# Performance work log

Measured on AMD Instinct MI355X. Metric: run time of the kernel, lower is better.

Reference implementation:

```python
import jax, jax.numpy as jnp
import numpy as np

B, C, H, W = 2, 512, 64, 64
NUM_HEADS = 8
HEAD_DIM = C // NUM_HEADS


def setup_inputs() -> dict:
    key = jax.random.key(0)
    ks = jax.random.split(key, 6)
    s = 1.0 / np.sqrt(C)
    return {
        "x": jax.random.normal(ks[0], (B, C, H, W), dtype=jnp.float32),
        "w_qkv": jax.random.normal(ks[1], (3 * C, C), dtype=jnp.float32) * s,
        "b_qkv": jax.random.normal(ks[2], (3 * C,), dtype=jnp.float32) * 0.01,
        "w_out": jax.random.normal(ks[3], (C, C), dtype=jnp.float32) * s,
        "b_out": jax.random.normal(ks[4], (C,), dtype=jnp.float32) * 0.01,
        "gamma": jax.random.normal(ks[5], (1,), dtype=jnp.float32) * 0.1,
    }


def reference(x, w_qkv, b_qkv, w_out, b_out, gamma):
    b, c, h, w = x.shape
    n = h * w
    nh, hd = NUM_HEADS, HEAD_DIM
    # 1x1 conv QKV projection == per-pixel linear
    qkv = jnp.einsum('oc,bchw->bohw', w_qkv, x) + b_qkv[None, :, None, None]
    qkv = qkv.reshape(b, 3, nh, hd, n)  # [B,3,nh,hd,N]
    q = qkv[:, 0].transpose(0, 1, 3, 2)  # [B,nh,N,hd]
    k = qkv[:, 1]                        # [B,nh,hd,N]
    v = qkv[:, 2].transpose(0, 1, 3, 2)  # [B,nh,N,hd]
    scale = hd ** -0.5
    attn = jnp.einsum('bhnd,bhdm->bhnm', q, k) * scale  # [B,nh,N,N]
    attn = jax.nn.softmax(attn, axis=-1)
    out = jnp.einsum('bhnm,bhmd->bhnd', attn, v)  # [B,nh,N,hd]
    out = out.transpose(0, 1, 3, 2).reshape(b, c, h, w)  # [B,C,H,W]
    out = jnp.einsum('oc,bchw->bohw', w_out, out) + b_out[None, :, None, None]
    return gamma[0] * out + x
```

## Files before the change

kernel.cpp:

```cpp
#include <hip/hip_runtime.h>
#include <hip/hip_bf16.h>

typedef __bf16 bf16_t;
typedef __bf16 bf16x8 __attribute__((ext_vector_type(8)));
typedef __bf16 bf16x4 __attribute__((ext_vector_type(4)));
typedef float floatx4 __attribute__((ext_vector_type(4)));
typedef float f32x16 __attribute__((ext_vector_type(16)));

#define MFMA_BF16(a, b, c) __builtin_amdgcn_mfma_f32_16x16x32_bf16((a), (b), (c), 0, 0, 0)
#define MFMA32(a, b, c) __builtin_amdgcn_mfma_f32_32x32x16_bf16((a), (b), (c), 0, 0, 0)

static constexpr int CB = 512;
static constexpr int NB = 4096;

__device__ __forceinline__ unsigned cvtpk_bf16(float lo, float hi_) {
  unsigned r;
  asm("v_cvt_pk_bf16_f32 %0, %1, %2" : "=v"(r) : "v"(lo), "v"(hi_));
  return r;
}
__device__ __forceinline__ void plswap(unsigned& x, unsigned& y) {
  asm volatile("v_permlane32_swap_b32 %0, %1" : "+v"(x), "+v"(y));
}
__device__ __forceinline__ float exp2_fast(float x) {
  float r;
  asm("v_exp_f32 %0, %1" : "=v"(r) : "v"(x));
  return r;
}

#define GLOAD_LDS16(gsrc, ldst)                                              \
  __builtin_amdgcn_global_load_lds(                                          \
      (const __attribute__((address_space(1))) void*)(gsrc),                 \
      (__attribute__((address_space(3))) void*)(ldst), 16, 0, 0)

__global__ __launch_bounds__(256) void k_qkv(const float* __restrict__ W,
                                             const float* __restrict__ bias,
                                             const float* __restrict__ x,
                                             bf16_t* __restrict__ Qb,
                                             bf16_t* __restrict__ Kb,
                                             bf16_t* __restrict__ Vb) {
  __shared__ __align__(16) bf16_t As[128 * 40];
  __shared__ __align__(16) bf16_t Bs[128 * 40];
  const int t = threadIdx.x;
  const int lane = t & 63, wv = t >> 6;
  const int g = lane >> 4, c = lane & 15;
  const int wm = wv >> 1, wn = wv & 1;
  const int o0 = blockIdx.x * 128, n0 = blockIdx.y * 128;
  const int b = blockIdx.z;

  floatx4 acc[4][4] = {};

  const float* Ap = W + (size_t)o0 * CB;
  const float* xb = x + (size_t)b * CB * NB + n0;

  for (int kt = 0; kt < CB; kt += 32) {
    {
      const int row = t >> 3, c4 = (t & 7) * 4;
#pragma unroll
      for (int p = 0; p < 4; ++p) {
        const int r = row + p * 32;
        const float4 v = *reinterpret_cast<const float4*>(Ap + (size_t)r * CB + kt + c4);
        bf16x4 w4;
        w4[0] = (bf16_t)v.x; w4[1] = (bf16_t)v.y; w4[2] = (bf16_t)v.z; w4[3] = (bf16_t)v.w;
        *reinterpret_cast<bf16x4*>(&As[r * 40 + c4]) = w4;
      }
    }
    {
      const int p2 = (t & 15) * 2;
      const int nq0 = t >> 4;
      const float* xr0 = xb + (size_t)(kt + p2) * NB;
      const float* xr1 = xr0 + NB;
#pragma unroll
      for (int it = 0; it < 2; ++it) {
        const int nn = (nq0 + 16 * it) * 4;
        const float4 a = *reinterpret_cast<const float4*>(xr0 + nn);
        const float4 bv = *reinterpret_cast<const float4*>(xr1 + nn);
        const unsigned u0 = cvtpk_bf16(a.x, bv.x);
        const unsigned u1 = cvtpk_bf16(a.y, bv.y);
        const unsigned u2 = cvtpk_bf16(a.z, bv.z);
        const unsigned u3 = cvtpk_bf16(a.w, bv.w);
        *reinterpret_cast<unsigned*>(&Bs[(nn + 0) * 40 + p2]) = u0;
        *reinterpret_cast<unsigned*>(&Bs[(nn + 1) * 40 + p2]) = u1;
        *reinterpret_cast<unsigned*>(&Bs[(nn + 2) * 40 + p2]) = u2;
        *reinterpret_cast<unsigned*>(&Bs[(nn + 3) * 40 + p2]) = u3;
      }
    }
    __syncthreads();
    bf16x8 af[4], bfr[4];
#pragma unroll
    for (int i = 0; i < 4; ++i)
      af[i] = *reinterpret_cast<const bf16x8*>(&As[(wm * 64 + i * 16 + c) * 40 + g * 8]);
#pragma unroll
    for (int j = 0; j < 4; ++j)
      bfr[j] = *reinterpret_cast<const bf16x8*>(&Bs[(wn * 64 + j * 16 + c) * 40 + g * 8]);
#pragma unroll
    for (int i = 0; i < 4; ++i)
#pragma unroll
      for (int j = 0; j < 4; ++j)
        acc[i][j] = MFMA_BF16(af[i], bfr[j], acc[i][j]);
    __syncthreads();
  }

  const int which = o0 >> 9;
#pragma unroll
  for (int i = 0; i < 4; ++i) {
    const int ob = o0 + wm * 64 + i * 16 + 4 * g;
    float bias4[4];
#pragma unroll
    for (int r = 0; r < 4; ++r) bias4[r] = bias[ob + r];
    const int h = (ob >> 6) & 7;
    const int d0 = ob & 63;
#pragma unroll
    for (int j = 0; j < 4; ++j) {
      const int n = n0 + wn * 64 + j * 16 + c;
      if (which == 2) {
        bf16_t* vp = Vb + (size_t)(b * 8 + h) * 64 * NB + n;
#pragma unroll
        for (int r = 0; r < 4; ++r)
          vp[(size_t)(d0 + r) * NB] = (bf16_t)(acc[i][j][r] + bias4[r]);
      } else {
        bf16_t* qp = (which == 0 ? Qb : Kb) + ((size_t)(b * 8 + h) * NB + n) * 64 + d0;
        bf16x4 pk;
#pragma unroll
        for (int r = 0; r < 4; ++r) pk[r] = (bf16_t)(acc[i][j][r] + bias4[r]);
        *reinterpret_cast<bf16x4*>(qp) = pk;
      }
    }
  }
}

__global__ __launch_bounds__(256, 2) void k_attn(const bf16_t* __restrict__ Qb,
                                                 const bf16_t* __restrict__ Kb,
                                                 const bf16_t* __restrict__ Vb,
                                                 bf16_t* __restrict__ P0,
                                                 bf16_t* __restrict__ P1,
                                                 float* __restrict__ lsum) {
  __shared__ __align__(16) bf16_t Kl[2][2][4096];
  __shared__ __align__(16) bf16_t Vl[2][2][4096];
  const int t = threadIdx.x, lane = t & 63, w = t >> 6;
  const int q31 = lane & 31, hi = lane >> 5;

  const int bid = blockIdx.x;
  const int xcd = bid & 7, j = bid >> 3;
  const int bh = xcd * 2 + (j >> 6);
  const int rest = j & 63;
  const int qt = rest >> 1, half = rest & 1;
  const int q0 = qt * 128 + w * 32;
  const int kvbase = half * 2048;

  const size_t base = (size_t)bh * NB * 64;
  const bf16_t* Qp = Qb + base;
  const bf16_t* Kp = Kb + base;
  const bf16_t* Vp = Vb + base;
  bf16_t* Op = (half ? P1 : P0) + base;

  const float SC = 0.125f * 1.44269504088896340736f;
  const float FM = 8.0f;

  bf16x8 qf[4];
#pragma unroll
  for (int ks = 0; ks < 4; ++ks) {
    bf16x8 q = *reinterpret_cast<const bf16x8*>(Qp + (size_t)(q0 + q31) * 64 + ks * 16 + hi * 8);
#pragma unroll
    for (int e = 0; e < 8; ++e) q[e] = (bf16_t)((float)q[e] * SC);
    qf[ks] = q;
  }

  bf16x8 ones;
#pragma unroll
  for (int e = 0; e < 8; ++e) ones[e] = (bf16_t)1.0f;

  const int srow0 = t >> 3, srow1 = srow0 + 32;
  const int sc0 = ((t & 7) ^ (srow0 & 7)) * 8;
  const int sc1 = ((t & 7) ^ (srow1 & 7)) * 8;
  const bf16_t* ksrc0 = Kp + (size_t)(kvbase + srow0) * 64 + sc0;
  const bf16_t* ksrc1 = Kp + (size_t)(kvbase + srow1) * 64 + sc1;
  const bf16_t* vsrc0 = Vp + (size_t)srow0 * NB + kvbase + sc0;
  const bf16_t* vsrc1 = Vp + (size_t)srow1 * NB + kvbase + sc1;

#define STAGE128(ss, bufi)                                                    \
  do {                                                                        \
    const size_t ko_ = (size_t)(ss) * 8192;                                   \
    const int vo_ = (ss) * 128;                                               \
    bf16_t* kd0_ = &Kl[(bufi)][0][0];                                         \
    bf16_t* kd1_ = &Kl[(bufi)][1][0];                                         \
    bf16_t* vd0_ = &Vl[(bufi)][0][0];                                         \
    bf16_t* vd1_ = &Vl[(bufi)][1][0];                                         \
    GLOAD_LDS16(ksrc0 + ko_, kd0_ + w * 512);                                 \
    GLOAD_LDS16(ksrc1 + ko_, kd0_ + 2048 + w * 512);                          \
    GLOAD_LDS16(ksrc0 + ko_ + 4096, kd1_ + w * 512);                          \
    GLOAD_LDS16(ksrc1 + ko_ + 4096, kd1_ + 2048 + w * 512);                   \
    GLOAD_LDS16(vsrc0 + vo_, vd0_ + w * 512);                                 \
    GLOAD_LDS16(vsrc1 + vo_, vd0_ + 2048 + w * 512);                         \
    GLOAD_LDS16(vsrc0 + vo_ + 64, vd1_ + w * 512);                            \
    GLOAD_LDS16(vsrc1 + vo_ + 64, vd1_ + 2048 + w * 512);                     \
  } while (0)

  int c16r[4];
#pragma unroll
  for (int ks = 0; ks < 4; ++ks) c16r[ks] = ((ks * 2 + hi) ^ (q31 & 7)) * 8;

  f32x16 O0 = {}, O1 = {}, lacc = {};
  f32x16 NEGM;
#pragma unroll
  for (int r = 0; r < 16; ++r) NEGM[r] = -FM;

  STAGE128(0, 0);
  asm volatile("s_waitcnt vmcnt(0)" ::: "memory");
  __builtin_amdgcn_s_barrier();
  __builtin_amdgcn_sched_barrier(0);

  int buf = 0;
  for (int s = 0; s < 16; ++s) {
    if (s < 15) STAGE128(s + 1, buf ^ 1);
#pragma unroll
    for (int sub = 0; sub < 2; ++sub) {
      const bf16_t* Kbuf = &Kl[buf][sub][0];
      const bf16_t* Vbuf = &Vl[buf][sub][0];
      f32x16 st0 = NEGM, st1 = NEGM;
      __builtin_amdgcn_s_setprio(1);
#pragma unroll
      for (int ks = 0; ks < 4; ++ks) {
        bf16x8 kf0 = *reinterpret_cast<const bf16x8*>(&Kbuf[q31 * 64 + c16r[ks]]);
        bf16x8 kf1 = *reinterpret_cast<const bf16x8*>(&Kbuf[(32 + q31) * 64 + c16r[ks]]);
        st0 = MFMA32(kf0, qf[ks], st0);
        st1 = MFMA32(kf1, qf[ks], st1);
      }
      __builtin_amdgcn_s_setprio(0);

#pragma unroll
      for (int r = 0; r < 16; ++r) st0[r] = exp2_fast(st0[r]);
#pragma unroll
      for (int r = 0; r < 16; ++r) st1[r] = exp2_fast(st1[r]);

      __builtin_amdgcn_s_setprio(1);
#pragma unroll
      for (int ks = 0; ks < 4; ++ks) {
        const f32x16& P = (ks < 2) ? st0 : st1;
        const int rb = (ks & 1) * 8;
        unsigned x0 = cvtpk_bf16(P[rb + 0], P[rb + 1]);
        unsigned y0 = cvtpk_bf16(P[rb + 4], P[rb + 5]);
        unsigned x1 = cvtpk_bf16(P[rb + 2], P[rb + 3]);
        unsigned y1 = cvtpk_bf16(P[rb + 6], P[rb + 7]);
        plswap(x0, y0);
        plswap(x1, y1);
        union { unsigned u[4]; bf16x8 v; } pa;
        pa.u[0] = x0; pa.u[1] = x1; pa.u[2] = y0; pa.u[3] = y1;
        bf16x8 vf0 = *reinterpret_cast<const bf16x8*>(&Vbuf[q31 * 64 + c16r[ks]]);
        bf16x8 vf1 = *reinterpret_cast<const bf16x8*>(&Vbuf[(32 + q31) * 64 + c16r[ks]]);
        O0 = MFMA32(pa.v, vf0, O0);
        O1 = MFMA32(pa.v, vf1, O1);
        lacc = MFMA32(pa.v, ones, lacc);
      }
      __builtin_amdgcn_s_setprio(0);
    }
    if (s < 15) {
      asm volatile("s_waitcnt vmcnt(0) lgkmcnt(0)" ::: "memory");
      __builtin_amdgcn_s_barrier();
      __builtin_amdgcn_sched_barrier(0);
    }
    buf ^= 1;
  }
#undef STAGE128

#pragma unroll
  for (int r = 0; r < 16; ++r) {
    const int n = q0 + (r & 3) + 8 * (r >> 2) + 4 * hi;
    bf16_t* op = Op + ((size_t)n) * 64 + q31;
    op[0]  = (bf16_t)O0[r];
    op[32] = (bf16_t)O1[r];
  }
  if (q31 == 0) {
    float* lp = lsum + (size_t)(half * 16 + bh) * NB;
#pragma unroll
    for (int r = 0; r < 16; ++r) {
      const int row = (r & 3) + 8 * (r >> 2) + 4 * hi;
      lp[q0 + row] = lacc[r];
    }
  }
}

__global__ __launch_bounds__(256) void k_out(const float* __restrict__ W,
                                             const float* __restrict__ bias,
                                             const bf16_t* __restrict__ P0,
                                             const bf16_t* __restrict__ P1,
                                             const float* __restrict__ lsum,
                                             const float* __restrict__ x,
                                             const float* __restrict__ gamma,
                                             float* __restrict__ y) {
  __shared__ __align__(16) bf16_t As[128 * 40];
  __shared__ __align__(16) bf16_t Bs[128 * 40];
  const int t = threadIdx.x;
  const int lane = t & 63, wv = t >> 6;
  const int g = lane >> 4, c = lane & 15;
  const int wm = wv >> 1, wn = wv & 1;
  const int o0 = blockIdx.x * 128, n0 = blockIdx.y * 128;
  const int b = blockIdx.z;

  floatx4 acc[4][4] = {};

  const float* Ap = W + (size_t)o0 * CB;

  for (int kt = 0; kt < CB; kt += 32) {
    {
      const int row = t >> 3, c4 = (t & 7) * 4;
#pragma unroll
      for (int p = 0; p < 4; ++p) {
        const int r = row + p * 32;
        const float4 v = *reinterpret_cast<const float4*>(Ap + (size_t)r * CB + kt + c4);
        bf16x4 w4;
        w4[0] = (bf16_t)v.x; w4[1] = (bf16_t)v.y; w4[2] = (bf16_t)v.z; w4[3] = (bf16_t)v.w;
        *reinterpret_cast<bf16x4*>(&As[r * 40 + c4]) = w4;
      }
    }
    {
      const int row = t >> 2, ch = t & 3;
      const int cc = kt + ch * 8;
      const int h = cc >> 6, d = cc & 63;
#pragma unroll
      for (int p = 0; p < 2; ++p) {
        const int r = row + p * 64;
        const int n = n0 + r;
        const size_t li = (size_t)(b * 8 + h) * NB + n;
        const size_t idx = li * 64 + d;
        const bf16x8 oa = *reinterpret_cast<const bf16x8*>(P0 + idx);
        const bf16x8 ob = *reinterpret_cast<const bf16x8*>(P1 + idx);
        const float rl = 1.0f / (lsum[li] + lsum[li + 16 * NB]);
        bf16x8 o;
#pragma unroll
        for (int e = 0; e < 8; ++e)
          o[e] = (bf16_t)(((float)oa[e] + (float)ob[e]) * rl);
        *reinterpret_cast<bf16x8*>(&Bs[r * 40 + ch * 8]) = o;
      }
    }
    __syncthreads();
    bf16x8 af[4], bfr[4];
#pragma unroll
    for (int i = 0; i < 4; ++i)
      af[i] = *reinterpret_cast<const bf16x8*>(&As[(wm * 64 + i * 16 + c) * 40 + g * 8]);
#pragma unroll
    for (int j = 0; j < 4; ++j)
      bfr[j] = *reinterpret_cast<const bf16x8*>(&Bs[(wn * 64 + j * 16 + c) * 40 + g * 8]);
#pragma unroll
    for (int i = 0; i < 4; ++i)
#pragma unroll
      for (int j = 0; j < 4; ++j)
        acc[i][j] = MFMA_BF16(af[i], bfr[j], acc[i][j]);
    __syncthreads();
  }

  const float gm = gamma[0];
#pragma unroll
  for (int i = 0; i < 4; ++i) {
    const int ob = o0 + wm * 64 + i * 16 + 4 * g;
    float bias4[4];
#pragma unroll
    for (int r = 0; r < 4; ++r) bias4[r] = bias[ob + r];
#pragma unroll
    for (int j = 0; j < 4; ++j) {
      const int n = n0 + wn * 64 + j * 16 + c;
      const float* xp = x + ((size_t)(b * CB + ob) * NB) + n;
      float* yp = y + ((size_t)(b * CB + ob) * NB) + n;
#pragma unroll
      for (int r = 0; r < 4; ++r)
        yp[(size_t)r * NB] = gm * (acc[i][j][r] + bias4[r]) + xp[(size_t)r * NB];
    }
  }
}

extern "C" void kernel_launch(void* const* d_in, const int* in_sizes, int n_in,
                              void* d_out, int out_size, void* d_ws, size_t ws_size,
                              hipStream_t stream) {
  const float* x      = (const float*)d_in[0];
  const float* w_qkv  = (const float*)d_in[1];
  const float* b_qkv  = (const float*)d_in[2];
  const float* w_out  = (const float*)d_in[3];
  const float* b_out  = (const float*)d_in[4];
  const float* gamma  = (const float*)d_in[5];
  float* y = (float*)d_out;

  const size_t CH = 4194304;
  bf16_t* Wp = (bf16_t*)d_ws;
  bf16_t* Qb = Wp;
  bf16_t* Kb = Wp + CH;
  bf16_t* Vb = Wp + 2 * CH;
  bf16_t* P0 = Wp + 3 * CH;
  bf16_t* P1 = Wp + 4 * CH;
  float*  lsum = (float*)(Wp + 5 * CH);

  k_qkv<<<dim3(12, 32, 2), 256, 0, stream>>>(w_qkv, b_qkv, x, Qb, Kb, Vb);
  k_attn<<<dim3(1024), 256, 0, stream>>>(Qb, Kb, Vb, P0, P1, lsum);
  k_out<<<dim3(4, 32, 2), 256, 0, stream>>>(w_out, b_out, P0, P1, lsum, x, gamma, y);
}
```

Baseline: 155.9 us.

## Pre-convert weights and transpose x to bf16, double-buffer QKV GEMM with direct LDS loads

Adds a kernel that converts both weight matrices to bf16 once per call and a kernel that transposes x into a bf16 [B,N,C] layout. The QKV GEMM then streams both operands with global_load_lds into double-buffered, XOR-swizzled LDS tiles with a K-step of 64, overlapping loads with MFMA work. The output projection also loads pre-converted bf16 weights directly into LDS. This removes per-tile fp32 loads and conversion from the GEMM inner loops, at the cost of two extra launches and extra workspace traffic. xT shares workspace with P0, which is safe only because k_qkv finishes before k_attn writes P0.

```diff
diff --git a/kernel.cpp b/kernel.cpp
--- a/kernel.cpp
+++ b/kernel.cpp
@@ -32,73 +32,124 @@
       (const __attribute__((address_space(1))) void*)(gsrc),                 \
       (__attribute__((address_space(3))) void*)(ldst), 16, 0, 0)
 
-__global__ __launch_bounds__(256) void k_qkv(const float* __restrict__ W,
-                                             const float* __restrict__ bias,
-                                             const float* __restrict__ x,
-                                             bf16_t* __restrict__ Qb,
-                                             bf16_t* __restrict__ Kb,
-                                             bf16_t* __restrict__ Vb) {
-  __shared__ __align__(16) bf16_t As[128 * 40];
-  __shared__ __align__(16) bf16_t Bs[128 * 40];
+__global__ __launch_bounds__(256) void k_cvtw(const float* __restrict__ w_qkv,
+                                              const float* __restrict__ w_out,
+                                              bf16_t* __restrict__ Wb,
+                                              bf16_t* __restrict__ Wo) {
+  const int idx = (blockIdx.x * 256 + threadIdx.x) * 8;
+  const float* src;
+  bf16_t* dst;
+  if (idx < 786432) { src = w_qkv + idx; dst = Wb + idx; }
+  else              { src = w_out + (idx - 786432); dst = Wo + (idx - 786432); }
+  const float4 a = *reinterpret_cast<const float4*>(src);
+  const float4 b = *reinterpret_cast<const float4*>(src + 4);
+  union { unsigned u[4]; bf16x8 v; } o;
+  o.u[0] = cvtpk_bf16(a.x, a.y);
+  o.u[1] = cvtpk_bf16(a.z, a.w);
+  o.u[2] = cvtpk_bf16(b.x, b.y);
+  o.u[3] = cvtpk_bf16(b.z, b.w);
+  *reinterpret_cast<bf16x8*>(dst) = o.v;
+}
+
+__global__ __launch_bounds__(256) void k_transpose(const float* __restrict__ x,
+                                                   bf16_t* __restrict__ xT) {
+  __shared__ __align__(16) bf16_t T[64 * 72];
   const int t = threadIdx.x;
-  const int lane = t & 63, wv = t >> 6;
+  const int b = blockIdx.z, c0 = blockIdx.y * 64, n0 = blockIdx.x * 64;
+  {
+    const int cl = t >> 4, nl = (t & 15) * 4;
+#pragma unroll
+    for (int p = 0; p < 4; ++p) {
+      const int c = cl + p * 16;
+      const float4 v = *reinterpret_cast<const float4*>(
+          x + ((size_t)(b * CB + c0 + c) * NB) + n0 + nl);
+      T[(nl + 0) * 72 + c] = (bf16_t)v.x;
+      T[(nl + 1) * 72 + c] = (bf16_t)v.y;
+      T[(nl + 2) * 72 + c] = (bf16_t)v.z;
+      T[(nl + 3) * 72 + c] = (bf16_t)v.w;
+    }
+  }
+  __syncthreads();
+  {
+    const int nr = t >> 2, ch = t & 3;
+    bf16_t* op = xT + ((size_t)(b * NB + n0 + nr) * CB) + c0;
+#pragma unroll
+    for (int p = 0; p < 2; ++p) {
+      bf16x8 v = *reinterpret_cast<const bf16x8*>(&T[nr * 72 + ch * 8 + p * 32]);
+      *reinterpret_cast<bf16x8*>(op + ch * 8 + p * 32) = v;
+    }
+  }
+}
+
+__global__ __launch_bounds__(256, 2) void k_qkv(const bf16_t* __restrict__ Wb,
+                                                const float* __restrict__ bias,
+                                                const bf16_t* __restrict__ xT,
+                                                bf16_t* __restrict__ Qb,
+                                                bf16_t* __restrict__ Kb,
+                                                bf16_t* __restrict__ Vb) {
+  __shared__ __align__(16) bf16_t As[2][128 * 64];
+  __shared__ __align__(16) bf16_t Bs[2][128 * 64];
+  const int t = threadIdx.x, lane = t & 63, w = t >> 6;
   const int g = lane >> 4, c = lane & 15;
-  const int wm = wv >> 1, wn = wv & 1;
+  const int wm = w >> 1, wn = w & 1;
   const int o0 = blockIdx.x * 128, n0 = blockIdx.y * 128;
   const int b = blockIdx.z;
 
   floatx4 acc[4][4] = {};
 
-  const float* Ap = W + (size_t)o0 * CB;
-  const float* xb = x + (size_t)b * CB * NB + n0;
-
-  for (int kt = 0; kt < CB; kt += 32) {
-    {
-      const int row = t >> 3, c4 = (t & 7) * 4;
-#pragma unroll
-      for (int p = 0; p < 4; ++p) {
-        const int r = row + p * 32;
-        const float4 v = *reinterpret_cast<const float4*>(Ap + (size_t)r * CB + kt + c4);
-        bf16x4 w4;
-        w4[0] = (bf16_t)v.x; w4[1] = (bf16_t)v.y; w4[2] = (bf16_t)v.z; w4[3] = (bf16_t)v.w;
-        *reinterpret_cast<bf16x4*>(&As[r * 40 + c4]) = w4;
-      }
-    }
-    {
-      const int p2 = (t & 15) * 2;
-      const int nq0 = t >> 4;
-      const float* xr0 = xb + (size_t)(kt + p2) * NB;
-      const float* xr1 = xr0 + NB;
-#pragma unroll
-      for (int it = 0; it < 2; ++it) {
-        const int nn = (nq0 + 16 * it) * 4;
-        const float4 a = *reinterpret_cast<const float4*>(xr0 + nn);
-        const float4 bv = *reinterpret_cast<const float4*>(xr1 + nn);
-        const unsigned u0 = cvtpk_bf16(a.x, bv.x);
-        const unsigned u1 = cvtpk_bf16(a.y, bv.y);
-        const unsigned u2 = cvtpk_bf16(a.z, bv.z);
-        const unsigned u3 = cvtpk_bf16(a.w, bv.w);
-        *reinterpret_cast<unsigned*>(&Bs[(nn + 0) * 40 + p2]) = u0;
-        *reinterpret_cast<unsigned*>(&Bs[(nn + 1) * 40 + p2]) = u1;
-        *reinterpret_cast<unsigned*>(&Bs[(nn + 2) * 40 + p2]) = u2;
-        *reinterpret_cast<unsigned*>(&Bs[(nn + 3) * 40 + p2]) = u3;
-      }
-    }
-    __syncthreads();
-    bf16x8 af[4], bfr[4];
-#pragma unroll
-    for (int i = 0; i < 4; ++i)
-      af[i] = *reinterpret_cast<const bf16x8*>(&As[(wm * 64 + i * 16 + c) * 40 + g * 8]);
-#pragma unroll
-    for (int j = 0; j < 4; ++j)
-      bfr[j] = *reinterpret_cast<const bf16x8*>(&Bs[(wn * 64 + j * 16 + c) * 40 + g * 8]);
-#pragma unroll
-    for (int i = 0; i < 4; ++i)
+  const int srow = t >> 3;
+  const int gch = (t & 7) ^ (srow & 7);
+  const bf16_t* asrc = Wb + (size_t)(o0 + srow) * CB + gch * 8;
+  const bf16_t* bsrc = xT + ((size_t)(b * NB + n0 + srow)) * CB + gch * 8;
+
+#define QSTAGE(kt_, bufi)                                                     \
+  do {                                                                        \
+    _Pragma("unroll")                                                         \
+    for (int p = 0; p < 4; ++p) {                                             \
+      GLOAD_LDS16(asrc + (size_t)p * 32 * CB + (kt_),                         \
+                  &As[(bufi)][w * 512 + p * 2048]);                           \
+      GLOAD_LDS16(bsrc + (size_t)p * 32 * CB + (kt_),                         \
+                  &Bs[(bufi)][w * 512 + p * 2048]);                           \
+    }                                                                         \
+  } while (0)
+
+  int cho[2];
+  cho[0] = (g ^ (c & 7)) * 8;
+  cho[1] = ((4 + g) ^ (c & 7)) * 8;
+
+  QSTAGE(0, 0);
+  asm volatile("s_waitcnt vmcnt(0)" ::: "memory");
+  __builtin_amdgcn_s_barrier();
+  __builtin_amdgcn_sched_barrier(0);
+
+  int buf = 0;
+  for (int s = 0; s < 8; ++s) {
+    if (s < 7) QSTAGE((s + 1) * 64, buf ^ 1);
+#pragma unroll
+    for (int ksub = 0; ksub < 2; ++ksub) {
+      bf16x8 af[4], bfr[4];
+#pragma unroll
+      for (int i = 0; i < 4; ++i)
+        af[i] = *reinterpret_cast<const bf16x8*>(
+            &As[buf][(wm * 64 + i * 16 + c) * 64 + cho[ksub]]);
 #pragma unroll
       for (int j = 0; j < 4; ++j)
-        acc[i][j] = MFMA_BF16(af[i], bfr[j], acc[i][j]);
-    __syncthreads();
-  }
+        bfr[j] = *reinterpret_cast<const bf16x8*>(
+            &Bs[buf][(wn * 64 + j * 16 + c) * 64 + cho[ksub]]);
+#pragma unroll
+      for (int i = 0; i < 4; ++i)
+#pragma unroll
+        for (int j = 0; j < 4; ++j)
+          acc[i][j] = MFMA_BF16(af[i], bfr[j], acc[i][j]);
+    }
+    if (s < 7) {
+      asm volatile("s_waitcnt vmcnt(0) lgkmcnt(0)" ::: "memory");
+      __builtin_amdgcn_s_barrier();
+      __builtin_amdgcn_sched_barrier(0);
+      buf ^= 1;
+    }
+  }
+#undef QSTAGE
 
   const int which = o0 >> 9;
 #pragma unroll
@@ -190,7 +241,7 @@
     GLOAD_LDS16(ksrc0 + ko_ + 4096, kd1_ + w * 512);                          \
     GLOAD_LDS16(ksrc1 + ko_ + 4096, kd1_ + 2048 + w * 512);                   \
     GLOAD_LDS16(vsrc0 + vo_, vd0_ + w * 512);                                 \
-    GLOAD_LDS16(vsrc1 + vo_, vd0_ + 2048 + w * 512);                         \
+    GLOAD_LDS16(vsrc1 + vo_, vd0_ + 2048 + w * 512);                          \
     GLOAD_LDS16(vsrc0 + vo_ + 64, vd1_ + w * 512);                            \
     GLOAD_LDS16(vsrc1 + vo_ + 64, vd1_ + 2048 + w * 512);                     \
   } while (0)
@@ -279,7 +330,7 @@
   }
 }
 
-__global__ __launch_bounds__(256) void k_out(const float* __restrict__ W,
+__global__ __launch_bounds__(256) void k_out(const bf16_t* __restrict__ Wo,
                                              const float* __restrict__ bias,
                                              const bf16_t* __restrict__ P0,
                                              const bf16_t* __restrict__ P1,
@@ -287,30 +338,26 @@
                                              const float* __restrict__ x,
                                              const float* __restrict__ gamma,
                                              float* __restrict__ y) {
-  __shared__ __align__(16) bf16_t As[128 * 40];
+  __shared__ __align__(16) bf16_t As[128 * 64];
   __shared__ __align__(16) bf16_t Bs[128 * 40];
   const int t = threadIdx.x;
-  const int lane = t & 63, wv = t >> 6;
+  const int lane = t & 63, w = t >> 6;
   const int g = lane >> 4, c = lane & 15;
-  const int wm = wv >> 1, wn = wv & 1;
+  const int wm = w >> 1, wn = w & 1;
   const int o0 = blockIdx.x * 128, n0 = blockIdx.y * 128;
   const int b = blockIdx.z;
 
   floatx4 acc[4][4] = {};
 
-  const float* Ap = W + (size_t)o0 * CB;
+  const int srow = t >> 3;
+  const int gch = (t & 7) ^ (srow & 7);
+  const bf16_t* asrc = Wo + (size_t)(o0 + srow) * CB + gch * 8;
 
   for (int kt = 0; kt < CB; kt += 32) {
-    {
-      const int row = t >> 3, c4 = (t & 7) * 4;
-#pragma unroll
-      for (int p = 0; p < 4; ++p) {
-        const int r = row + p * 32;
-        const float4 v = *reinterpret_cast<const float4*>(Ap + (size_t)r * CB + kt + c4);
-        bf16x4 w4;
-        w4[0] = (bf16_t)v.x; w4[1] = (bf16_t)v.y; w4[2] = (bf16_t)v.z; w4[3] = (bf16_t)v.w;
-        *reinterpret_cast<bf16x4*>(&As[r * 40 + c4]) = w4;
-      }
+    if ((kt & 63) == 0) {
+#pragma unroll
+      for (int p = 0; p < 4; ++p)
+        GLOAD_LDS16(asrc + (size_t)p * 32 * CB + kt, &As[w * 512 + p * 2048]);
     }
     {
       const int row = t >> 2, ch = t & 3;
@@ -333,10 +380,12 @@
       }
     }
     __syncthreads();
+    const int ksub = (kt >> 5) & 1;
+    const int acho = ((ksub * 4 + g) ^ (c & 7)) * 8;
     bf16x8 af[4], bfr[4];
 #pragma unroll
     for (int i = 0; i < 4; ++i)
-      af[i] = *reinterpret_cast<const bf16x8*>(&As[(wm * 64 + i * 16 + c) * 40 + g * 8]);
+      af[i] = *reinterpret_cast<const bf16x8*>(&As[(wm * 64 + i * 16 + c) * 64 + acho]);
 #pragma unroll
     for (int j = 0; j < 4; ++j)
       bfr[j] = *reinterpret_cast<const bf16x8*>(&Bs[(wn * 64 + j * 16 + c) * 40 + g * 8]);
@@ -383,11 +432,16 @@
   bf16_t* Qb = Wp;
   bf16_t* Kb = Wp + CH;
   bf16_t* Vb = Wp + 2 * CH;
-  bf16_t* P0 = Wp + 3 * CH;
-  bf16_t* P1 = Wp + 4 * CH;
-  float*  lsum = (float*)(Wp + 5 * CH);
-
-  k_qkv<<<dim3(12, 32, 2), 256, 0, stream>>>(w_qkv, b_qkv, x, Qb, Kb, Vb);
+  bf16_t* P1 = Wp + 3 * CH;
+  bf16_t* xT = Wp + 4 * CH;
+  bf16_t* P0 = Wp + 4 * CH;
+  bf16_t* Wb = Wp + 5 * CH;
+  bf16_t* Wo = Wb + 786432;
+  float*  lsum = (float*)(Wo + 262144);
+
+  k_cvtw<<<dim3(512), 256, 0, stream>>>(w_qkv, w_out, Wb, Wo);
+  k_transpose<<<dim3(64, 8, 2), 256, 0, stream>>>(x, xT);
+  k_qkv<<<dim3(12, 32, 2), 256, 0, stream>>>(Wb, b_qkv, xT, Qb, Kb, Vb);
   k_attn<<<dim3(1024), 256, 0, stream>>>(Qb, Kb, Vb, P0, P1, lsum);
-  k_out<<<dim3(4, 32, 2), 256, 0, stream>>>(w_out, b_out, P0, P1, lsum, x, gamma, y);
-}
+  k_out<<<dim3(4, 32, 2), 256, 0, stream>>>(Wo, b_out, P0, P1, lsum, x, gamma, y);
+}
```

After: 148.4 us. 4.8% less time.
